# Kernel optimization log

Measured on AMD Instinct MI355X. Metric: run time of the kernel, lower is better.

Reference implementation:

```python
import jax, jax.numpy as jnp
import numpy as np

B, S, D, H, E = 8, 196, 768, 12, 8
HD = D // H  # 64
FF = 4 * D   # 3072
EPS = 1e-5


def setup_inputs() -> dict:
    key = jax.random.key(0)
    ks = jax.random.split(key, 12)
    s = 0.02
    inp = {
        'x': jax.random.normal(ks[0], (B, S, D), jnp.float32),
        'ln1_g': jnp.ones((D,), jnp.float32),
        'ln1_b': jnp.zeros((D,), jnp.float32),
        'Wq': jax.random.normal(ks[1], (D, D), jnp.float32) * s,
        'bq': jnp.zeros((D,), jnp.float32),
        'Wk': jax.random.normal(ks[2], (D, HD), jnp.float32) * s,
        'bk': jnp.zeros((HD,), jnp.float32),
        'Wv': jax.random.normal(ks[3], (D, HD), jnp.float32) * s,
        'bv': jnp.zeros((HD,), jnp.float32),
        'ln2_g': jnp.ones((D,), jnp.float32),
        'ln2_b': jnp.zeros((D,), jnp.float32),
        'Wg': jax.random.normal(ks[4], (D, E), jnp.float32) * s,
        'bg': jnp.zeros((E,), jnp.float32),
        'W1': jax.random.normal(ks[5], (E, D, FF), jnp.float32) * s,
        'b1': jnp.zeros((E, FF), jnp.float32),
        'W2': jax.random.normal(ks[6], (E, FF, D), jnp.float32) * s,
        'b2': jnp.zeros((E, D), jnp.float32),
    }
    return inp


def _layernorm(x, g, b):
    mu = jnp.mean(x, axis=-1, keepdims=True)
    var = jnp.var(x, axis=-1, keepdims=True)
    return (x - mu) * jax.lax.rsqrt(var + EPS) * g + b


def _rotate_half(x):
    x1, x2 = jnp.split(x, 2, axis=-1)
    return jnp.concatenate((-x2, x1), axis=-1)


def _rope(seq_len):
    inv_freq = 1.0 / (10000.0 ** (jnp.arange(0, HD, 2, dtype=jnp.float32) / HD))
    freqs = jnp.arange(seq_len, dtype=jnp.float32)[:, None] * inv_freq[None, :]
    emb = jnp.concatenate((freqs, freqs), axis=-1)  # [S, HD]
    return emb[None, :, None, :]  # [1, S, 1, HD]


def _attention(x, Wq, bq, Wk, bk, Wv, bv):
    b, s, _ = x.shape
    q = (x @ Wq + bq).reshape(b, s, H, HD)
    k = (x @ Wk + bk).reshape(b, s, 1, HD)
    v = (x @ Wv + bv).reshape(b, s, 1, HD)
    k = jnp.broadcast_to(k, (b, s, H, HD))
    v = jnp.broadcast_to(v, (b, s, H, HD))
    pe = _rope(s)
    cos, sin = jnp.cos(pe), jnp.sin(pe)
    q = q * cos + _rotate_half(q) * sin
    k = k * cos + _rotate_half(k) * sin
    scale = HD ** -0.5
    # NOTE: faithful to source -- matmul over the last two dims of [b,s,h,d],
    # i.e. attention across HEADS, not sequence positions.
    attn = jnp.einsum('bshd,bsgd->bshg', q, k) * scale
    attn = jax.nn.softmax(attn, axis=-1)
    out = jnp.einsum('bshg,bsgd->bshd', attn, v)
    return out.reshape(b, s, H * HD)


def _moe(x, Wg, bg, W1, b1, W2, b2):
    b, s, d = x.shape
    xt = x.reshape(-1, d)  # [T, D]
    gates = jax.nn.softmax(xt @ Wg + bg, axis=-1)
    top1 = jnp.argmax(gates, axis=-1)  # topk(k=2)[:,0] == argmax
    out = jnp.zeros_like(xt)
    for e in range(E):  # small fixed expert count
        h = jax.nn.gelu(xt @ W1[e] + b1[e], approximate=False)
        y = h @ W2[e] + b2[e]
        out = jnp.where((top1 == e)[:, None], y, out)
    return out.reshape(b, s, d)


def reference(x, ln1_g, ln1_b, Wq, bq, Wk, bk, Wv, bv, ln2_g, ln2_b, Wg, bg, W1, b1, W2, b2):
    res = x
    h = _layernorm(x, ln1_g, ln1_b)
    h = _attention(h, Wq, bq, Wk, bk, Wv, bv)
    x = res + h
    res = x
    h = _layernorm(x, ln2_g, ln2_b)
    h = _moe(h, Wg, bg, W1, b1, W2, b2)
    return res + h
```

## Files before the change

### kernel.cpp

```cpp
#include <hip/hip_runtime.h>


typedef unsigned short u16;
typedef short bf16x8_t __attribute__((ext_vector_type(8)));
typedef short bf16x4_t __attribute__((ext_vector_type(4)));
typedef float f32x4_t  __attribute__((ext_vector_type(4)));

#define T_TOK 1568
#define DM 768
#define HD 64
#define FF 3072
#define NE 8

#define OFF_CNT   0
#define OFF_N12   32
#define OFF_ITEM1 64
#define OFF_ITEM2 864
#define OFF_BUCK  4096
#define OFF_H2    54272
#define OFF_HMID  2462720

__device__ __forceinline__ float bf2f(u16 h) {
    unsigned u = ((unsigned)h) << 16;
    return __builtin_bit_cast(float, u);
}
__device__ __forceinline__ u16 f2bf(float f) {
    unsigned u = __builtin_bit_cast(unsigned, f);
    unsigned r = (u + 0x7FFFu + ((u >> 16) & 1u)) >> 16;
    return (u16)r;
}
__device__ __forceinline__ float gelu_f(float x) {
    return 0.5f * x * (1.0f + erff(x * 0.70710678118654752440f));
}

__global__ __launch_bounds__(256) void k_pre(
        const float* __restrict__ x,
        const float* __restrict__ g1, const float* __restrict__ b1,
        const float* __restrict__ Wv, const float* __restrict__ bv,
        const float* __restrict__ g2, const float* __restrict__ b2g,
        const float* __restrict__ Wg, const float* __restrict__ bg,
        const float* __restrict__ b2moe,
        u16* __restrict__ h2, float* __restrict__ out,
        int* __restrict__ cnt, int* __restrict__ buck) {
    __shared__ __align__(16) u16 h1s[8 * DM];
    __shared__ float wgs[NE * DM];
    __shared__ float g2s[DM], b2s[DM];
    __shared__ float ps[4 * 8 * 64];
    __shared__ float vsm[8 * 64];
    int tid = threadIdx.x, lane = tid & 63, w = tid >> 6;
    int tb = blockIdx.x * 8;

    for (int idx = tid; idx < NE * DM; idx += 256) {
        int e = idx / DM, c = idx % DM;
        wgs[idx] = Wg[(size_t)c * NE + e];
    }
    for (int idx = tid; idx < DM; idx += 256) { g2s[idx] = g2[idx]; b2s[idx] = b2g[idx]; }

    float xv[2][12];
#pragma unroll
    for (int ttl = 0; ttl < 2; ttl++) {
        int tl = w * 2 + ttl;
        int t = tb + tl;
        const float* xp = x + (size_t)t * DM;
        float s = 0.0f;
#pragma unroll
        for (int i = 0; i < 12; i++) { float q = xp[lane + 64 * i]; xv[ttl][i] = q; s += q; }
#pragma unroll
        for (int m = 1; m < 64; m <<= 1) s += __shfl_xor(s, m);
        float mu = s * (1.0f / DM);
        float vs = 0.0f;
#pragma unroll
        for (int i = 0; i < 12; i++) { float d = xv[ttl][i] - mu; vs += d * d; }
#pragma unroll
        for (int m = 1; m < 64; m <<= 1) vs += __shfl_xor(vs, m);
        float rs = rsqrtf(vs * (1.0f / DM) + 1e-5f);
#pragma unroll
        for (int i = 0; i < 12; i++) {
            int c = lane + 64 * i;
            h1s[tl * DM + c] = f2bf((xv[ttl][i] - mu) * rs * g1[c] + b1[c]);
        }
    }
    __syncthreads();

    float acc[8];
#pragma unroll
    for (int tt = 0; tt < 8; tt++) acc[tt] = 0.0f;
    const float* wp = Wv + (size_t)(w * 192) * HD + lane;
    for (int kk = 0; kk < 192; kk += 4) {
        float w0 = wp[(size_t)(kk + 0) * HD];
        float w1 = wp[(size_t)(kk + 1) * HD];
        float w2 = wp[(size_t)(kk + 2) * HD];
        float w3 = wp[(size_t)(kk + 3) * HD];
        int kb = w * 192 + kk;
#pragma unroll
        for (int tt = 0; tt < 8; tt++) {
            bf16x4_t hh = *(const bf16x4_t*)&h1s[tt * DM + kb];
            acc[tt] += bf2f((u16)hh[0]) * w0 + bf2f((u16)hh[1]) * w1 +
                       bf2f((u16)hh[2]) * w2 + bf2f((u16)hh[3]) * w3;
        }
    }
#pragma unroll
    for (int tt = 0; tt < 8; tt++) ps[(w * 8 + tt) * 64 + lane] = acc[tt];
    __syncthreads();
#pragma unroll
    for (int s2 = 0; s2 < 2; s2++) {
        int tt = w * 2 + s2;
        vsm[tt * 64 + lane] = ps[tt * 64 + lane] + ps[(8 + tt) * 64 + lane] +
                              ps[(16 + tt) * 64 + lane] + ps[(24 + tt) * 64 + lane] +
                              bv[lane];
    }
    __syncthreads();

#pragma unroll
    for (int ttl = 0; ttl < 2; ttl++) {
        int tl = w * 2 + ttl;
        int t = tb + tl;
        float vl = vsm[tl * 64 + lane];
        float x2v[12];
        float s = 0.0f;
#pragma unroll
        for (int i = 0; i < 12; i++) { float q = xv[ttl][i] + vl; x2v[i] = q; s += q; }
#pragma unroll
        for (int m = 1; m < 64; m <<= 1) s += __shfl_xor(s, m);
        float mu = s * (1.0f / DM);
        float vs = 0.0f;
#pragma unroll
        for (int i = 0; i < 12; i++) { float d = x2v[i] - mu; vs += d * d; }
#pragma unroll
        for (int m = 1; m < 64; m <<= 1) vs += __shfl_xor(vs, m);
        float rs = rsqrtf(vs * (1.0f / DM) + 1e-5f);
        float le[NE];
#pragma unroll
        for (int e = 0; e < NE; e++) le[e] = 0.0f;
        u16* h2p = h2 + (size_t)t * DM;
#pragma unroll
        for (int i = 0; i < 12; i++) {
            int c = lane + 64 * i;
            float h = (x2v[i] - mu) * rs * g2s[c] + b2s[c];
            h2p[c] = f2bf(h);
#pragma unroll
            for (int e = 0; e < NE; e++) le[e] += h * wgs[e * DM + c];
        }
#pragma unroll
        for (int e = 0; e < NE; e++) {
#pragma unroll
            for (int m = 1; m < 64; m <<= 1) le[e] += __shfl_xor(le[e], m);
        }
        float best = le[0] + bg[0]; int be = 0;
#pragma unroll
        for (int e = 1; e < NE; e++) {
            float q = le[e] + bg[e];
            if (q > best) { best = q; be = e; }
        }
        if (lane == 0) {
            int pos = atomicAdd(&cnt[be], 1);
            buck[be * T_TOK + pos] = t;
        }
        float* op = out + (size_t)t * DM;
        const float* bp = b2moe + (size_t)be * DM;
#pragma unroll
        for (int i = 0; i < 12; i++) {
            int c = lane + 64 * i;
            op[c] = x2v[i] + bp[c];
        }
    }
}

__global__ void k_plan(const int* __restrict__ cnt, int* __restrict__ n12,
                       int* __restrict__ item1, int* __restrict__ item2) {
    if (threadIdx.x == 0) {
        int n1 = 0, n2 = 0;
        for (int e = 0; e < NE; e++) {
            int mts = (cnt[e] + 63) >> 6;
            for (int mt = 0; mt < mts; mt++) {
                int code = e * 64 + mt;
                item1[n1++] = code;
                for (int kc = 0; kc < 4; kc++) item2[n2++] = code * 4 + kc;
            }
        }
        n12[0] = n1; n12[1] = n2;
    }
}

__global__ __launch_bounds__(256) void k_moe_gemm1(
        const u16* __restrict__ h2, const float* __restrict__ W1,
        const float* __restrict__ b1, const int* __restrict__ cnt,
        const int* __restrict__ n12, const int* __restrict__ item1,
        const int* __restrict__ buck, u16* __restrict__ hmid) {
    int nt = blockIdx.x, n0 = nt * 64;
    int n1 = n12[0];
    int tid = threadIdx.x, lane = tid & 63, wid = tid >> 6;
    int arow = tid >> 3, ac = tid & 7;
    int bn = tid & 63, bkg = tid >> 6;
    int lr = lane & 15, q = lane >> 4;
    __shared__ __align__(16) u16 As[64 * 72];
    __shared__ __align__(16) u16 Bs[64 * 72];

    for (int it = blockIdx.y; it < n1; it += gridDim.y) {
        int code = item1[it];
        int e = code >> 6, mt = code & 63;
        int cnte = cnt[e], m0 = mt * 64;
        const float* W1e = W1 + (size_t)e * DM * FF;
        int atok[2];
#pragma unroll
        for (int j = 0; j < 2; j++) {
            int i = m0 + arow + 32 * j;
            atok[j] = (i < cnte) ? buck[e * T_TOK + i] : -1;
        }
        f32x4_t acc[4];
#pragma unroll
        for (int ni = 0; ni < 4; ni++) acc[ni] = (f32x4_t){0.f, 0.f, 0.f, 0.f};

        bf16x8_t a_pre[2];
        float b_pre[16];
#pragma unroll
        for (int j = 0; j < 2; j++) {
            bf16x8_t v = {0, 0, 0, 0, 0, 0, 0, 0};
            if (atok[j] >= 0) v = *(const bf16x8_t*)&h2[(size_t)atok[j] * DM + ac * 8];
            a_pre[j] = v;
        }
        {
            const float* bp = W1e + (size_t)(bkg * 16) * FF + n0 + bn;
#pragma unroll
            for (int kk = 0; kk < 16; kk++) b_pre[kk] = bp[(size_t)kk * FF];
        }
        const int NK = DM / 64;
        for (int kt = 0; kt < NK; kt++) {
            __syncthreads();
#pragma unroll
            for (int j = 0; j < 2; j++)
                *(bf16x8_t*)&As[(arow + 32 * j) * 72 + ac * 8] = a_pre[j];
            {
                bf16x8_t p0, p1;
#pragma unroll
                for (int kk = 0; kk < 8; kk++) {
                    p0[kk] = (short)f2bf(b_pre[kk]);
                    p1[kk] = (short)f2bf(b_pre[kk + 8]);
                }
                *(bf16x8_t*)&Bs[bn * 72 + bkg * 16] = p0;
                *(bf16x8_t*)&Bs[bn * 72 + bkg * 16 + 8] = p1;
            }
            __syncthreads();
            if (kt + 1 < NK) {
                int k0 = (kt + 1) * 64;
#pragma unroll
                for (int j = 0; j < 2; j++) {
                    bf16x8_t v = {0, 0, 0, 0, 0, 0, 0, 0};
                    if (atok[j] >= 0)
                        v = *(const bf16x8_t*)&h2[(size_t)atok[j] * DM + k0 + ac * 8];
                    a_pre[j] = v;
                }
                const float* bp = W1e + (size_t)(k0 + bkg * 16) * FF + n0 + bn;
#pragma unroll
                for (int kk = 0; kk < 16; kk++) b_pre[kk] = bp[(size_t)kk * FF];
            }
#pragma unroll
            for (int s = 0; s < 2; s++) {
                bf16x8_t af = *(const bf16x8_t*)&As[(wid * 16 + lr) * 72 + s * 32 + q * 8];
#pragma unroll
                for (int ni = 0; ni < 4; ni++) {
                    bf16x8_t bfr = *(const bf16x8_t*)&Bs[(ni * 16 + lr) * 72 + s * 32 + q * 8];
                    acc[ni] = __builtin_amdgcn_mfma_f32_16x16x32_bf16(af, bfr, acc[ni], 0, 0, 0);
                }
            }
        }
        float bias[4];
#pragma unroll
        for (int ni = 0; ni < 4; ni++) bias[ni] = b1[(size_t)e * FF + n0 + ni * 16 + lr];
#pragma unroll
        for (int r = 0; r < 4; r++) {
            int i = m0 + wid * 16 + q * 4 + r;
            if (i < cnte) {
                int t = buck[e * T_TOK + i];
                size_t base = (size_t)t * FF + n0;
#pragma unroll
                for (int ni = 0; ni < 4; ni++)
                    hmid[base + ni * 16 + lr] = f2bf(gelu_f(acc[ni][r] + bias[ni]));
            }
        }
    }
}

__global__ __launch_bounds__(256) void k_moe_gemm2(
        const u16* __restrict__ hmid, const float* __restrict__ W2,
        const int* __restrict__ cnt, const int* __restrict__ n12,
        const int* __restrict__ item2, const int* __restrict__ buck,
        float* __restrict__ out) {
    int nt = blockIdx.x, n0 = nt * 64;
    int n2 = n12[1];
    int tid = threadIdx.x, lane = tid & 63, wid = tid >> 6;
    int arow = tid >> 3, ac = tid & 7;
    int bn = tid & 63, bkg = tid >> 6;
    int lr = lane & 15, q = lane >> 4;
    __shared__ __align__(16) u16 As[64 * 72];
    __shared__ __align__(16) u16 Bs[64 * 72];

    for (int it = blockIdx.y; it < n2; it += gridDim.y) {
        int code2 = item2[it];
        int kc = code2 & 3, code = code2 >> 2;
        int e = code >> 6, mt = code & 63;
        int cnte = cnt[e], m0 = mt * 64;
        int kbase = kc * (FF / 4);
        const float* W2e = W2 + (size_t)e * FF * DM;
        int atok[2];
#pragma unroll
        for (int j = 0; j < 2; j++) {
            int i = m0 + arow + 32 * j;
            atok[j] = (i < cnte) ? buck[e * T_TOK + i] : -1;
        }
        f32x4_t acc[4];
#pragma unroll
        for (int ni = 0; ni < 4; ni++) acc[ni] = (f32x4_t){0.f, 0.f, 0.f, 0.f};

        bf16x8_t a_pre[2];
        float b_pre[16];
#pragma unroll
        for (int j = 0; j < 2; j++) {
            bf16x8_t v = {0, 0, 0, 0, 0, 0, 0, 0};
            if (atok[j] >= 0)
                v = *(const bf16x8_t*)&hmid[(size_t)atok[j] * FF + kbase + ac * 8];
            a_pre[j] = v;
        }
        {
            const float* bp = W2e + (size_t)(kbase + bkg * 16) * DM + n0 + bn;
#pragma unroll
            for (int kk = 0; kk < 16; kk++) b_pre[kk] = bp[(size_t)kk * DM];
        }
        const int NK = (FF / 4) / 64;
        for (int kt = 0; kt < NK; kt++) {
            __syncthreads();
#pragma unroll
            for (int j = 0; j < 2; j++)
                *(bf16x8_t*)&As[(arow + 32 * j) * 72 + ac * 8] = a_pre[j];
            {
                bf16x8_t p0, p1;
#pragma unroll
                for (int kk = 0; kk < 8; kk++) {
                    p0[kk] = (short)f2bf(b_pre[kk]);
                    p1[kk] = (short)f2bf(b_pre[kk + 8]);
                }
                *(bf16x8_t*)&Bs[bn * 72 + bkg * 16] = p0;
                *(bf16x8_t*)&Bs[bn * 72 + bkg * 16 + 8] = p1;
            }
            __syncthreads();
            if (kt + 1 < NK) {
                int k0 = kbase + (kt + 1) * 64;
#pragma unroll
                for (int j = 0; j < 2; j++) {
                    bf16x8_t v = {0, 0, 0, 0, 0, 0, 0, 0};
                    if (atok[j] >= 0)
                        v = *(const bf16x8_t*)&hmid[(size_t)atok[j] * FF + k0 + ac * 8];
                    a_pre[j] = v;
                }
                const float* bp = W2e + (size_t)(k0 + bkg * 16) * DM + n0 + bn;
#pragma unroll
                for (int kk = 0; kk < 16; kk++) b_pre[kk] = bp[(size_t)kk * DM];
            }
#pragma unroll
            for (int s = 0; s < 2; s++) {
                bf16x8_t af = *(const bf16x8_t*)&As[(wid * 16 + lr) * 72 + s * 32 + q * 8];
#pragma unroll
                for (int ni = 0; ni < 4; ni++) {
                    bf16x8_t bfr = *(const bf16x8_t*)&Bs[(ni * 16 + lr) * 72 + s * 32 + q * 8];
                    acc[ni] = __builtin_amdgcn_mfma_f32_16x16x32_bf16(af, bfr, acc[ni], 0, 0, 0);
                }
            }
        }
#pragma unroll
        for (int r = 0; r < 4; r++) {
            int i = m0 + wid * 16 + q * 4 + r;
            if (i < cnte) {
                int t = buck[e * T_TOK + i];
                size_t base = (size_t)t * DM + n0;
#pragma unroll
                for (int ni = 0; ni < 4; ni++)
                    atomicAdd(&out[base + ni * 16 + lr], acc[ni][r]);
            }
        }
    }
}

extern "C" void kernel_launch(void* const* d_in, const int* in_sizes, int n_in,
                              void* d_out, int out_size, void* d_ws, size_t ws_size,
                              hipStream_t stream) {
    const float* x    = (const float*)d_in[0];
    const float* ln1g = (const float*)d_in[1];
    const float* ln1b = (const float*)d_in[2];
    const float* Wv   = (const float*)d_in[7];
    const float* bv   = (const float*)d_in[8];
    const float* ln2g = (const float*)d_in[9];
    const float* ln2b = (const float*)d_in[10];
    const float* Wg   = (const float*)d_in[11];
    const float* bg   = (const float*)d_in[12];
    const float* W1   = (const float*)d_in[13];
    const float* b1   = (const float*)d_in[14];
    const float* W2   = (const float*)d_in[15];
    const float* b2   = (const float*)d_in[16];

    char* ws = (char*)d_ws;
    int*   cnt   = (int*)(ws + OFF_CNT);
    int*   n12   = (int*)(ws + OFF_N12);
    int*   item1 = (int*)(ws + OFF_ITEM1);
    int*   item2 = (int*)(ws + OFF_ITEM2);
    int*   buck  = (int*)(ws + OFF_BUCK);
    u16*   h2    = (u16*)(ws + OFF_H2);
    u16*   hmid  = (u16*)(ws + OFF_HMID);
    float* out   = (float*)d_out;

    hipMemsetAsync(cnt, 0, 16 * sizeof(int), stream);
    k_pre<<<T_TOK / 8, 256, 0, stream>>>(x, ln1g, ln1b, Wv, bv, ln2g, ln2b,
                                         Wg, bg, b2, h2, out, cnt, buck);
    k_plan<<<1, 64, 0, stream>>>(cnt, n12, item1, item2);
    k_moe_gemm1<<<dim3(FF / 64, 32), 256, 0, stream>>>(h2, W1, b1, cnt, n12,
                                                       item1, buck, hmid);
    k_moe_gemm2<<<dim3(DM / 64, 128), 256, 0, stream>>>(hmid, W2, cnt, n12,
                                                        item2, buck, out);
}
```

Before: 321.8 us.

## Enlarge MoE GEMM tiles to 128x128 with K-step 32 and 2x8 MFMA per wave

Both expert GEMM kernels move from 64x64 output tiles with K-step 64 to 128x128 tiles with K-step 32. Each wave now computes a 32x128 slab of 2x8 MFMA accumulators, reusing each A fragment across 8 B fragments and each B fragment across 2 A fragments. The LDS row stride shrinks to 44 elements, and the planning kernel and grid sizes are updated for 128-row tiles. This cuts redundant fp32 weight reads and conversions per output element and raises MFMA density. In exchange it uses more accumulator registers, halves the K work per barrier, and launches fewer blocks, which can leave tiles underfilled for small experts.

Result: no change. 322.6 us (+0.2%).

```diff
diff --git a/kernel.cpp b/kernel.cpp
--- a/kernel.cpp
+++ b/kernel.cpp
@@ -11,6 +11,7 @@
 #define HD 64
 #define FF 3072
 #define NE 8
+#define LDSW 44
 
 #define OFF_CNT   0
 #define OFF_N12   32
@@ -171,7 +172,7 @@
     if (threadIdx.x == 0) {
         int n1 = 0, n2 = 0;
         for (int e = 0; e < NE; e++) {
-            int mts = (cnt[e] + 63) >> 6;
+            int mts = (cnt[e] + 127) >> 7;
             for (int mt = 0; mt < mts; mt++) {
                 int code = e * 64 + mt;
                 item1[n1++] = code;
@@ -187,29 +188,31 @@
         const float* __restrict__ b1, const int* __restrict__ cnt,
         const int* __restrict__ n12, const int* __restrict__ item1,
         const int* __restrict__ buck, u16* __restrict__ hmid) {
-    int nt = blockIdx.x, n0 = nt * 64;
+    int nt = blockIdx.x, n0 = nt * 128;
     int n1 = n12[0];
     int tid = threadIdx.x, lane = tid & 63, wid = tid >> 6;
-    int arow = tid >> 3, ac = tid & 7;
-    int bn = tid & 63, bkg = tid >> 6;
+    int arow = tid >> 2, ac = tid & 3;
+    int bn = tid & 127, bkg = tid >> 7;
     int lr = lane & 15, q = lane >> 4;
-    __shared__ __align__(16) u16 As[64 * 72];
-    __shared__ __align__(16) u16 Bs[64 * 72];
+    __shared__ __align__(16) u16 As[128 * LDSW];
+    __shared__ __align__(16) u16 Bs[128 * LDSW];
 
     for (int it = blockIdx.y; it < n1; it += gridDim.y) {
         int code = item1[it];
         int e = code >> 6, mt = code & 63;
-        int cnte = cnt[e], m0 = mt * 64;
+        int cnte = cnt[e], m0 = mt * 128;
         const float* W1e = W1 + (size_t)e * DM * FF;
         int atok[2];
 #pragma unroll
         for (int j = 0; j < 2; j++) {
-            int i = m0 + arow + 32 * j;
+            int i = m0 + arow + 64 * j;
             atok[j] = (i < cnte) ? buck[e * T_TOK + i] : -1;
         }
-        f32x4_t acc[4];
-#pragma unroll
-        for (int ni = 0; ni < 4; ni++) acc[ni] = (f32x4_t){0.f, 0.f, 0.f, 0.f};
+        f32x4_t acc[2][8];
+#pragma unroll
+        for (int mi = 0; mi < 2; mi++)
+#pragma unroll
+            for (int ni = 0; ni < 8; ni++) acc[mi][ni] = (f32x4_t){0.f, 0.f, 0.f, 0.f};
 
         bf16x8_t a_pre[2];
         float b_pre[16];
@@ -224,12 +227,12 @@
 #pragma unroll
             for (int kk = 0; kk < 16; kk++) b_pre[kk] = bp[(size_t)kk * FF];
         }
-        const int NK = DM / 64;
+        const int NK = DM / 32;
         for (int kt = 0; kt < NK; kt++) {
             __syncthreads();
 #pragma unroll
             for (int j = 0; j < 2; j++)
-                *(bf16x8_t*)&As[(arow + 32 * j) * 72 + ac * 8] = a_pre[j];
+                *(bf16x8_t*)&As[(arow + 64 * j) * LDSW + ac * 8] = a_pre[j];
             {
                 bf16x8_t p0, p1;
 #pragma unroll
@@ -237,12 +240,12 @@
                     p0[kk] = (short)f2bf(b_pre[kk]);
                     p1[kk] = (short)f2bf(b_pre[kk + 8]);
                 }
-                *(bf16x8_t*)&Bs[bn * 72 + bkg * 16] = p0;
-                *(bf16x8_t*)&Bs[bn * 72 + bkg * 16 + 8] = p1;
+                *(bf16x8_t*)&Bs[bn * LDSW + bkg * 16] = p0;
+                *(bf16x8_t*)&Bs[bn * LDSW + bkg * 16 + 8] = p1;
             }
             __syncthreads();
             if (kt + 1 < NK) {
-                int k0 = (kt + 1) * 64;
+                int k0 = (kt + 1) * 32;
 #pragma unroll
                 for (int j = 0; j < 2; j++) {
                     bf16x8_t v = {0, 0, 0, 0, 0, 0, 0, 0};
@@ -254,28 +257,33 @@
 #pragma unroll
                 for (int kk = 0; kk < 16; kk++) b_pre[kk] = bp[(size_t)kk * FF];
             }
-#pragma unroll
-            for (int s = 0; s < 2; s++) {
-                bf16x8_t af = *(const bf16x8_t*)&As[(wid * 16 + lr) * 72 + s * 32 + q * 8];
-#pragma unroll
-                for (int ni = 0; ni < 4; ni++) {
-                    bf16x8_t bfr = *(const bf16x8_t*)&Bs[(ni * 16 + lr) * 72 + s * 32 + q * 8];
-                    acc[ni] = __builtin_amdgcn_mfma_f32_16x16x32_bf16(af, bfr, acc[ni], 0, 0, 0);
-                }
-            }
-        }
-        float bias[4];
-#pragma unroll
-        for (int ni = 0; ni < 4; ni++) bias[ni] = b1[(size_t)e * FF + n0 + ni * 16 + lr];
-#pragma unroll
-        for (int r = 0; r < 4; r++) {
-            int i = m0 + wid * 16 + q * 4 + r;
-            if (i < cnte) {
-                int t = buck[e * T_TOK + i];
-                size_t base = (size_t)t * FF + n0;
-#pragma unroll
-                for (int ni = 0; ni < 4; ni++)
-                    hmid[base + ni * 16 + lr] = f2bf(gelu_f(acc[ni][r] + bias[ni]));
+            bf16x8_t af[2];
+#pragma unroll
+            for (int mi = 0; mi < 2; mi++)
+                af[mi] = *(const bf16x8_t*)&As[(wid * 32 + mi * 16 + lr) * LDSW + q * 8];
+#pragma unroll
+            for (int ni = 0; ni < 8; ni++) {
+                bf16x8_t bfr = *(const bf16x8_t*)&Bs[(ni * 16 + lr) * LDSW + q * 8];
+#pragma unroll
+                for (int mi = 0; mi < 2; mi++)
+                    acc[mi][ni] = __builtin_amdgcn_mfma_f32_16x16x32_bf16(af[mi], bfr, acc[mi][ni], 0, 0, 0);
+            }
+        }
+        float bias[8];
+#pragma unroll
+        for (int ni = 0; ni < 8; ni++) bias[ni] = b1[(size_t)e * FF + n0 + ni * 16 + lr];
+#pragma unroll
+        for (int mi = 0; mi < 2; mi++) {
+#pragma unroll
+            for (int r = 0; r < 4; r++) {
+                int i = m0 + wid * 32 + mi * 16 + q * 4 + r;
+                if (i < cnte) {
+                    int t = buck[e * T_TOK + i];
+                    size_t base = (size_t)t * FF + n0;
+#pragma unroll
+                    for (int ni = 0; ni < 8; ni++)
+                        hmid[base + ni * 16 + lr] = f2bf(gelu_f(acc[mi][ni][r] + bias[ni]));
+                }
             }
         }
     }
@@ -286,31 +294,33 @@
         const int* __restrict__ cnt, const int* __restrict__ n12,
         const int* __restrict__ item2, const int* __restrict__ buck,
         float* __restrict__ out) {
-    int nt = blockIdx.x, n0 = nt * 64;
+    int nt = blockIdx.x, n0 = nt * 128;
     int n2 = n12[1];
     int tid = threadIdx.x, lane = tid & 63, wid = tid >> 6;
-    int arow = tid >> 3, ac = tid & 7;
-    int bn = tid & 63, bkg = tid >> 6;
+    int arow = tid >> 2, ac = tid & 3;
+    int bn = tid & 127, bkg = tid >> 7;
     int lr = lane & 15, q = lane >> 4;
-    __shared__ __align__(16) u16 As[64 * 72];
-    __shared__ __align__(16) u16 Bs[64 * 72];
+    __shared__ __align__(16) u16 As[128 * LDSW];
+    __shared__ __align__(16) u16 Bs[128 * LDSW];
 
     for (int it = blockIdx.y; it < n2; it += gridDim.y) {
         int code2 = item2[it];
         int kc = code2 & 3, code = code2 >> 2;
         int e = code >> 6, mt = code & 63;
-        int cnte = cnt[e], m0 = mt * 64;
+        int cnte = cnt[e], m0 = mt * 128;
         int kbase = kc * (FF / 4);
         const float* W2e = W2 + (size_t)e * FF * DM;
         int atok[2];
 #pragma unroll
         for (int j = 0; j < 2; j++) {
-            int i = m0 + arow + 32 * j;
+            int i = m0 + arow + 64 * j;
             atok[j] = (i < cnte) ? buck[e * T_TOK + i] : -1;
         }
-        f32x4_t acc[4];
-#pragma unroll
-        for (int ni = 0; ni < 4; ni++) acc[ni] = (f32x4_t){0.f, 0.f, 0.f, 0.f};
+        f32x4_t acc[2][8];
+#pragma unroll
+        for (int mi = 0; mi < 2; mi++)
+#pragma unroll
+            for (int ni = 0; ni < 8; ni++) acc[mi][ni] = (f32x4_t){0.f, 0.f, 0.f, 0.f};
 
         bf16x8_t a_pre[2];
         float b_pre[16];
@@ -326,12 +336,12 @@
 #pragma unroll
             for (int kk = 0; kk < 16; kk++) b_pre[kk] = bp[(size_t)kk * DM];
         }
-        const int NK = (FF / 4) / 64;
+        const int NK = (FF / 4) / 32;
         for (int kt = 0; kt < NK; kt++) {
             __syncthreads();
 #pragma unroll
             for (int j = 0; j < 2; j++)
-                *(bf16x8_t*)&As[(arow + 32 * j) * 72 + ac * 8] = a_pre[j];
+                *(bf16x8_t*)&As[(arow + 64 * j) * LDSW + ac * 8] = a_pre[j];
             {
                 bf16x8_t p0, p1;
 #pragma unroll
@@ -339,12 +349,12 @@
                     p0[kk] = (short)f2bf(b_pre[kk]);
                     p1[kk] = (short)f2bf(b_pre[kk + 8]);
                 }
-                *(bf16x8_t*)&Bs[bn * 72 + bkg * 16] = p0;
-                *(bf16x8_t*)&Bs[bn * 72 + bkg * 16 + 8] = p1;
+                *(bf16x8_t*)&Bs[bn * LDSW + bkg * 16] = p0;
+                *(bf16x8_t*)&Bs[bn * LDSW + bkg * 16 + 8] = p1;
             }
             __syncthreads();
             if (kt + 1 < NK) {
-                int k0 = kbase + (kt + 1) * 64;
+                int k0 = kbase + (kt + 1) * 32;
 #pragma unroll
                 for (int j = 0; j < 2; j++) {
                     bf16x8_t v = {0, 0, 0, 0, 0, 0, 0, 0};
@@ -356,25 +366,30 @@
 #pragma unroll
                 for (int kk = 0; kk < 16; kk++) b_pre[kk] = bp[(size_t)kk * DM];
             }
-#pragma unroll
-            for (int s = 0; s < 2; s++) {
-                bf16x8_t af = *(const bf16x8_t*)&As[(wid * 16 + lr) * 72 + s * 32 + q * 8];
-#pragma unroll
-                for (int ni = 0; ni < 4; ni++) {
-                    bf16x8_t bfr = *(const bf16x8_t*)&Bs[(ni * 16 + lr) * 72 + s * 32 + q * 8];
-                    acc[ni] = __builtin_amdgcn_mfma_f32_16x16x32_bf16(af, bfr, acc[ni], 0, 0, 0);
-                }
-            }
-        }
-#pragma unroll
-        for (int r = 0; r < 4; r++) {
-            int i = m0 + wid * 16 + q * 4 + r;
-            if (i < cnte) {
-                int t = buck[e * T_TOK + i];
-                size_t base = (size_t)t * DM + n0;
-#pragma unroll
-                for (int ni = 0; ni < 4; ni++)
-                    atomicAdd(&out[base + ni * 16 + lr], acc[ni][r]);
+            bf16x8_t af[2];
+#pragma unroll
+            for (int mi = 0; mi < 2; mi++)
+                af[mi] = *(const bf16x8_t*)&As[(wid * 32 + mi * 16 + lr) * LDSW + q * 8];
+#pragma unroll
+            for (int ni = 0; ni < 8; ni++) {
+                bf16x8_t bfr = *(const bf16x8_t*)&Bs[(ni * 16 + lr) * LDSW + q * 8];
+#pragma unroll
+                for (int mi = 0; mi < 2; mi++)
+                    acc[mi][ni] = __builtin_amdgcn_mfma_f32_16x16x32_bf16(af[mi], bfr, acc[mi][ni], 0, 0, 0);
+            }
+        }
+#pragma unroll
+        for (int mi = 0; mi < 2; mi++) {
+#pragma unroll
+            for (int r = 0; r < 4; r++) {
+                int i = m0 + wid * 32 + mi * 16 + q * 4 + r;
+                if (i < cnte) {
+                    int t = buck[e * T_TOK + i];
+                    size_t base = (size_t)t * DM + n0;
+#pragma unroll
+                    for (int ni = 0; ni < 8; ni++)
+                        atomicAdd(&out[base + ni * 16 + lr], acc[mi][ni][r]);
+                }
             }
         }
     }
@@ -411,8 +426,8 @@
     k_pre<<<T_TOK / 8, 256, 0, stream>>>(x, ln1g, ln1b, Wv, bv, ln2g, ln2b,
                                          Wg, bg, b2, h2, out, cnt, buck);
     k_plan<<<1, 64, 0, stream>>>(cnt, n12, item1, item2);
-    k_moe_gemm1<<<dim3(FF / 64, 32), 256, 0, stream>>>(h2, W1, b1, cnt, n12,
-                                                       item1, buck, hmid);
-    k_moe_gemm2<<<dim3(DM / 64, 128), 256, 0, stream>>>(hmid, W2, cnt, n12,
+    k_moe_gemm1<<<dim3(FF / 128, 24), 256, 0, stream>>>(h2, W1, b1, cnt, n12,
+                                                        item1, buck, hmid);
+    k_moe_gemm2<<<dim3(DM / 128, 96), 256, 0, stream>>>(hmid, W2, cnt, n12,
                                                         item2, buck, out);
 }
```
